# Performance work log

Hardware: AMD Instinct MI355X
Metric: run time of the kernel (lower is better)

## Reference

```python
import jax, jax.numpy as jnp
import numpy as np

B, N, D, L, NREPEAT = 32, 577, 384, 12, 4
H = 4 * D  # mlp hidden
EPS = 1e-6


def ln(x, w, b):
    mu = jnp.mean(x, axis=-1, keepdims=True)
    var = jnp.mean(jnp.square(x - mu), axis=-1, keepdims=True)
    return (x - mu) * jax.lax.rsqrt(var + EPS) * w + b


def setup_inputs() -> dict:
    key = jax.random.key(0)
    ks = jax.random.split(key, 16)
    s = 0.02
    return {
        "x": jax.random.normal(ks[0], (B, N, D), dtype=jnp.float32),
        "norm1_w": jnp.ones((L, D), jnp.float32),
        "norm1_b": jnp.zeros((L, D), jnp.float32),
        "qkv_w": jax.random.normal(ks[1], (L, 3 * D, D), jnp.float32) * s,
        "qkv_b": jnp.zeros((L, 3 * D), jnp.float32),
        "qn_w": jnp.ones((L, D), jnp.float32),
        "qn_b": jnp.zeros((L, D), jnp.float32),
        "kn_w": jnp.ones((L, D), jnp.float32),
        "kn_b": jnp.zeros((L, D), jnp.float32),
        "an_w": jnp.ones((L, D), jnp.float32),
        "an_b": jnp.zeros((L, D), jnp.float32),
        "proj_w": jax.random.normal(ks[2], (L, D, D), jnp.float32) * s,
        "proj_b": jnp.zeros((L, D), jnp.float32),
        "ls1": jnp.full((L, D), 1e-5, jnp.float32),
        "norm2_w": jnp.ones((L, D), jnp.float32),
        "norm2_b": jnp.zeros((L, D), jnp.float32),
        "fc1_w": jax.random.normal(ks[3], (L, H, D), jnp.float32) * s,
        "fc1_b": jnp.zeros((L, H), jnp.float32),
        "fc2_w": jax.random.normal(ks[4], (L, D, H), jnp.float32) * s,
        "fc2_b": jnp.zeros((L, D), jnp.float32),
        "ls2": jnp.full((L, D), 1e-5, jnp.float32),
    }


def _forward(x, norm1_w, norm1_b, qkv_w, qkv_b, qn_w, qn_b, kn_w, kn_b,
             an_w, an_b, proj_w, proj_b, ls1, norm2_w, norm2_b,
             fc1_w, fc1_b, fc2_w, fc2_b, ls2):
    scale = 1.0 / np.sqrt(D).astype(np.float32)
    x_prime = x
    history = []  # list of [B, 1, D] cls tokens, grows each repeat
    for _ in range(NREPEAT):
        new_cls = x[:, 0:1]
        x = jnp.concatenate([new_cls, x_prime[:, 1:]], axis=1)  # [B, N, D]
        mem = jnp.concatenate([x] + history, axis=1)            # [B, N+t, D]
        for l in range(L):
            res1 = x
            xn = ln(x, norm1_w[l], norm1_b[l])
            # manual qkv split: q from normed x, k/v from UNNORMED mem
            q = xn @ qkv_w[l, :D].T + qkv_b[l, :D]
            k = mem @ qkv_w[l, D:2 * D].T + qkv_b[l, D:2 * D]
            v = mem @ qkv_w[l, 2 * D:].T + qkv_b[l, 2 * D:]
            q = ln(q, qn_w[l], qn_b[l])
            k = ln(k, kn_w[l], kn_b[l])
            # single-head SDPA over full width D
            attn = jax.nn.softmax(jnp.einsum('bqd,bkd->bqk', q, k) * scale, axis=-1)
            prod = jnp.einsum('bqk,bkd->bqd', attn, v)
            prod = ln(prod, an_w[l], an_b[l])
            proj = prod @ proj_w[l].T + proj_b[l]
            x = proj * ls1[l] + res1
            res2 = x
            x2 = ln(x, norm2_w[l], norm2_b[l])
            h = jax.nn.gelu(x2 @ fc1_w[l].T + fc1_b[l], approximate=False)
            x1 = h @ fc2_w[l].T + fc2_b[l]
            x = x1 * ls2[l] + res2
        history.append(new_cls)
    return x


def reference(x, norm1_w, norm1_b, qkv_w, qkv_b, qn_w, qn_b, kn_w, kn_b,
              an_w, an_b, proj_w, proj_b, ls1, norm2_w, norm2_b,
              fc1_w, fc1_b, fc2_w, fc2_b, ls2):
    return _forward(x, norm1_w, norm1_b, qkv_w, qkv_b, qn_w, qn_b, kn_w, kn_b,
                    an_w, an_b, proj_w, proj_b, ls1, norm2_w, norm2_b,
                    fc1_w, fc1_b, fc2_w, fc2_b, ls2)
```

## Files before the change

### kernel.cpp

```cpp
#include <hip/hip_runtime.h>
#include <math.h>

#define BB 32
#define NN 577
#define DD 384
#define HD 1536
#define LL 12
#define MP 608
#define NRPT 4

typedef __attribute__((ext_vector_type(8))) short bf16x8;
typedef __attribute__((ext_vector_type(4))) float f32x4;

__device__ __forceinline__ unsigned short f2bf(float f){
  unsigned u = __builtin_bit_cast(unsigned, f);
  u += 0x7fffu + ((u >> 16) & 1u);
  return (unsigned short)(u >> 16);
}
__device__ __forceinline__ float bf2f(unsigned short s){
  unsigned u = ((unsigned)s) << 16;
  return __builtin_bit_cast(float, u);
}

__device__ __forceinline__ void async16(void* lds, const void* g){
  __builtin_amdgcn_global_load_lds(
      (const __attribute__((address_space(1))) unsigned int*)g,
      (__attribute__((address_space(3))) unsigned int*)lds, 16, 0, 0);
}


__global__ void reset_k(float* __restrict__ x, const float* __restrict__ xp, float* __restrict__ cls){
  int i = blockIdx.x * 256 + threadIdx.x;
  if (i >= BB*NN*DD) return;
  int d = i % DD;
  int n = (i / DD) % NN;
  int b = i / (NN*DD);
  if (n == 0) cls[b*DD + d] = x[i];
  else x[i] = xp[i];
}

__global__ void fillmem_k(const float* __restrict__ x, const float* __restrict__ cls_hist,
                          unsigned short* __restrict__ mem, int r){
  int i = blockIdx.x * 256 + threadIdx.x;
  if (i >= BB*MP*DD) return;
  int d = i % DD;
  int n = (i / DD) % MP;
  int b = i / (MP*DD);
  float v = 0.f;
  if (n < NN) v = x[((size_t)b*NN + n)*DD + d];
  else if (n < NN + r) v = cls_hist[(size_t)(n-NN)*BB*DD + b*DD + d];
  mem[i] = f2bf(v);
}

__global__ void castL_k(const float* __restrict__ qkvw, const float* __restrict__ pw,
                        const float* __restrict__ f1w, const float* __restrict__ f2w,
                        unsigned short* __restrict__ wbuf){
  int i = blockIdx.x * 256 + threadIdx.x;
  const int QKV = 3*DD*DD;
  const int PRJ = DD*DD;
  const int F1  = HD*DD;
  const int TOT = QKV + PRJ + 2*F1;
  if (i >= TOT) return;
  float v;
  if (i < QKV) v = qkvw[i];
  else if (i < QKV+PRJ) v = pw[i-QKV];
  else if (i < QKV+PRJ+F1) v = f1w[i-QKV-PRJ];
  else v = f2w[i-QKV-PRJ-F1];
  wbuf[i] = f2bf(v);
}


template<typename T>
__global__ __launch_bounds__(64) void ln_k(const T* __restrict__ in, const float* __restrict__ w,
                                           const float* __restrict__ bias, unsigned short* __restrict__ out){
  int row = blockIdx.x;
  int lane = threadIdx.x;
  const T* p = in + (size_t)row*DD;
  float v[6];
  float s = 0.f;
  #pragma unroll
  for (int i=0;i<6;i++){
    float t;
    if (sizeof(T) == 4) t = (float)p[lane + i*64];
    else t = bf2f((unsigned short)p[lane + i*64]);
    v[i] = t; s += t;
  }
  #pragma unroll
  for (int o=32;o;o>>=1) s += __shfl_xor(s, o, 64);
  float mu = s * (1.f/DD);
  float q = 0.f;
  #pragma unroll
  for (int i=0;i<6;i++){ float t = v[i]-mu; q += t*t; }
  #pragma unroll
  for (int o=32;o;o>>=1) q += __shfl_xor(q, o, 64);
  float rs = rsqrtf(q*(1.f/DD) + 1e-6f);
  unsigned short* po = out + (size_t)row*DD;
  #pragma unroll
  for (int i=0;i<6;i++){
    int c = lane + i*64;
    po[c] = f2bf((v[i]-mu)*rs*w[c] + bias[c]);
  }
}


template<int EPI>
__global__ __launch_bounds__(256) void gemm128(
    const unsigned short* __restrict__ A, int lda, int arows, long sA,
    const unsigned short* __restrict__ B, int ldb, int brows, long sB,
    const float* __restrict__ bias,
    int K, int N,
    float* __restrict__ outF, unsigned short* __restrict__ outB,
    int ldo, int orows, long sO,
    const float* __restrict__ ls){

  __shared__ unsigned short a_sh[128*32];
  __shared__ unsigned short b_sh[128*32];

  int tid  = threadIdx.x;
  int wave = tid >> 6, lane = tid & 63;
  int lr = lane & 15, kg = lane >> 4;
  int wm = wave >> 1, wn = wave & 1;
  int z = blockIdx.z;
  int row0 = blockIdx.y * 128;
  int col0 = blockIdx.x * 128;

  const unsigned short* Ab = A + (size_t)z*sA;
  const unsigned short* Bb = B + (size_t)z*sB;

  f32x4 zf = {0.f,0.f,0.f,0.f};
  f32x4 acc[4][4];
  #pragma unroll
  for (int i=0;i<4;i++)
    #pragma unroll
    for (int j=0;j<4;j++) acc[i][j] = zf;

  int ra[2], rb[2], kc[2];
  #pragma unroll
  for (int it=0; it<2; it++){
    int c = tid + it*256;
    int r = row0 + (c>>2); if (r > arows-1) r = arows-1;
    ra[it] = r;
    r = col0 + (c>>2); if (r > brows-1) r = brows-1;
    rb[it] = r;
    kc[it] = (c&3)*8;
  }

  for (int k0 = 0; k0 < K; k0 += 32){
    #pragma unroll
    for (int it=0; it<2; it++){
      unsigned short* la = &a_sh[(it*256 + wave*64)*8];
      unsigned short* lb = &b_sh[(it*256 + wave*64)*8];
      async16(la, Ab + (size_t)ra[it]*lda + k0 + kc[it]);
      async16(lb, Bb + (size_t)rb[it]*ldb + k0 + kc[it]);
    }
    __syncthreads();
    bf16x8 af[4], bf[4];
    #pragma unroll
    for (int i=0;i<4;i++){
      af[i] = *(const bf16x8*)&a_sh[(wm*64 + i*16 + lr)*32 + kg*8];
      bf[i] = *(const bf16x8*)&b_sh[(wn*64 + i*16 + lr)*32 + kg*8];
    }
    #pragma unroll
    for (int i=0;i<4;i++)
      #pragma unroll
      for (int j=0;j<4;j++)
        acc[i][j] = __builtin_amdgcn_mfma_f32_16x16x32_bf16(af[i], bf[j], acc[i][j], 0,0,0);
    __syncthreads();
  }

  float* oF = outF ? outF + (size_t)z*sO : nullptr;
  unsigned short* oB = outB ? outB + (size_t)z*sO : nullptr;

  #pragma unroll
  for (int mi=0;mi<4;mi++)
    #pragma unroll
    for (int ni=0;ni<4;ni++)
      #pragma unroll
      for (int r=0;r<4;r++){
        int row = row0 + wm*64 + mi*16 + kg*4 + r;
        int col = col0 + wn*64 + ni*16 + lr;
        if (row >= orows || col >= N) continue;
        float vv = acc[mi][ni][r];
        size_t idx = (size_t)row*ldo + col;
        if (EPI == 0){
          if (bias) vv += bias[col];
          oB[idx] = f2bf(vv);
        } else if (EPI == 1){
          vv += bias[row];
          oB[idx] = f2bf(vv);
        } else if (EPI == 2){
          vv += bias[col];
          oF[idx] = vv*ls[col] + oF[idx];
        } else {
          vv += bias[col];
          float g = 0.5f*vv*(1.f + erff(vv*0.70710678118f));
          oB[idx] = f2bf(g);
        }
      }
}

__global__ __launch_bounds__(64) void softmax_k(const unsigned short* __restrict__ S,
                                                unsigned short* __restrict__ P, int M){
  int row = blockIdx.x;
  int m = row % MP;
  int lane = threadIdx.x;
  unsigned short* po = P + (size_t)row*MP;
  if (m >= NN){
    for (int n = lane; n < MP; n += 64) po[n] = 0;
    return;
  }
  const unsigned short* ps = S + (size_t)row*MP;
  const float scale = 0.05103103588f;
  float t[10];
  float mx = -INFINITY;
  #pragma unroll
  for (int i=0;i<10;i++){
    int n = lane + i*64;
    float v = (n < M) ? bf2f(ps[n])*scale : -INFINITY;
    t[i] = v; mx = fmaxf(mx, v);
  }
  #pragma unroll
  for (int o=32;o;o>>=1) mx = fmaxf(mx, __shfl_xor(mx, o, 64));
  float s = 0.f;
  #pragma unroll
  for (int i=0;i<10;i++){
    int n = lane + i*64;
    float e = (n < M) ? expf(t[i]-mx) : 0.f;
    t[i] = e; s += e;
  }
  #pragma unroll
  for (int o=32;o;o>>=1) s += __shfl_xor(s, o, 64);
  float inv = 1.f / s;
  #pragma unroll
  for (int i=0;i<10;i++){
    int n = lane + i*64;
    if (n < MP) po[n] = f2bf(t[i]*inv);
  }
}


extern "C" void kernel_launch(void* const* d_in, const int* in_sizes, int n_in,
                              void* d_out, int out_size, void* d_ws, size_t ws_size,
                              hipStream_t stream){
  const float* x_in = (const float*)d_in[0];
  const float* n1w  = (const float*)d_in[1];
  const float* n1b  = (const float*)d_in[2];
  const float* qkvw = (const float*)d_in[3];
  const float* qkvb = (const float*)d_in[4];
  const float* qnw  = (const float*)d_in[5];
  const float* qnb  = (const float*)d_in[6];
  const float* knw  = (const float*)d_in[7];
  const float* knb  = (const float*)d_in[8];
  const float* anw  = (const float*)d_in[9];
  const float* anb  = (const float*)d_in[10];
  const float* pw   = (const float*)d_in[11];
  const float* pb   = (const float*)d_in[12];
  const float* ls1  = (const float*)d_in[13];
  const float* n2w  = (const float*)d_in[14];
  const float* n2b  = (const float*)d_in[15];
  const float* f1w  = (const float*)d_in[16];
  const float* f1b  = (const float*)d_in[17];
  const float* f2w  = (const float*)d_in[18];
  const float* f2bb = (const float*)d_in[19];
  const float* ls2  = (const float*)d_in[20];

  char* ws = (char*)d_ws;
  size_t off = 0;
  auto alloc = [&](size_t bytes)->char* {
    char* p = ws + off;
    off = (off + bytes + 255) & ~(size_t)255;
    return p;
  };

  const int QKV = 3*DD*DD, PRJ = DD*DD, F1 = HD*DD;
  const size_t WTOT = (size_t)QKV + PRJ + 2*F1;
  const size_t SLOT = (size_t)BB*MP*DD;

  unsigned short* wbuf  = (unsigned short*)alloc(WTOT*2);
  float*          cls_h = (float*)         alloc((size_t)NRPT*BB*DD*4);
  unsigned short* mem_bf= (unsigned short*)alloc(SLOT*2);
  unsigned short* pool  = (unsigned short*)alloc(6*SLOT*2);

  unsigned short* wq = wbuf;
  unsigned short* wp = wbuf + QKV;
  unsigned short* w1 = wbuf + QKV + PRJ;
  unsigned short* w2 = wbuf + QKV + PRJ + F1;

  unsigned short* S0 = pool;
  unsigned short* S1 = pool + SLOT;
  unsigned short* S2 = pool + 2*SLOT;
  unsigned short* S3 = pool + 3*SLOT;
  unsigned short* S4 = pool + 4*SLOT;
  unsigned short* S5 = pool + 5*SLOT;

  unsigned short* xn    = S0;
  unsigned short* qraw  = S1;
  unsigned short* kraw  = S2;
  unsigned short* qb    = S3;
  unsigned short* kb    = S4;
  unsigned short* vT    = S5;
  unsigned short* Ssc   = S1;
  unsigned short* Pbf   = S3;
  unsigned short* prod  = S0;
  unsigned short* prodn = S1;
  unsigned short* x2    = S0;
  unsigned short* h     = S1;

  float* xf = (float*)d_out;

  auto cg = [](size_t n){ return dim3((unsigned)((n + 255) / 256)); };

  hipMemcpyAsync(xf, x_in, (size_t)BB*NN*DD*4, hipMemcpyDeviceToDevice, stream);

  const int RT  = (BB*NN + 127)/128;
  const int RTM = (BB*MP)/128;

  for (int r = 0; r < NRPT; r++){
    int M = NN + r;
    reset_k<<<cg((size_t)BB*NN*DD),256,0,stream>>>(xf, x_in, cls_h + (size_t)r*BB*DD);
    fillmem_k<<<cg((size_t)BB*MP*DD),256,0,stream>>>(xf, cls_h, mem_bf, r);
    for (int l = 0; l < LL; l++){
      castL_k<<<cg(WTOT),256,0,stream>>>(qkvw + (size_t)l*QKV, pw + (size_t)l*PRJ,
                                         f1w + (size_t)l*F1, f2w + (size_t)l*F1, wbuf);
      ln_k<float><<<BB*NN,64,0,stream>>>(xf, n1w + l*DD, n1b + l*DD, xn);
      gemm128<0><<<dim3(3,RT,1),256,0,stream>>>(xn,384,BB*NN,0, wq,384,384,0,
          qkvb + l*3*DD, 384,384, nullptr,qraw,384,BB*NN,0, nullptr);
      gemm128<0><<<dim3(3,RTM,1),256,0,stream>>>(mem_bf,384,BB*MP,0, wq + (size_t)DD*DD,384,384,0,
          qkvb + l*3*DD + DD, 384,384, nullptr,kraw,384,BB*MP,0, nullptr);
      gemm128<1><<<dim3(5,3,BB),256,0,stream>>>(wq + (size_t)2*DD*DD,384,384,0, mem_bf,384,MP,(long)MP*DD,
          qkvb + l*3*DD + 2*DD, 384,MP, nullptr,vT,MP,384,(long)DD*MP, nullptr);
      ln_k<unsigned short><<<BB*NN,64,0,stream>>>(qraw, qnw + l*DD, qnb + l*DD, qb);
      ln_k<unsigned short><<<BB*MP,64,0,stream>>>(kraw, knw + l*DD, knb + l*DD, kb);
      gemm128<0><<<dim3(5,5,BB),256,0,stream>>>(qb,384,NN,(long)NN*DD, kb,384,MP,(long)MP*DD,
          nullptr, 384,MP, nullptr,Ssc,MP,NN,(long)MP*MP, nullptr);
      softmax_k<<<BB*MP,64,0,stream>>>(Ssc, Pbf, M);
      gemm128<0><<<dim3(3,5,BB),256,0,stream>>>(Pbf,MP,MP,(long)MP*MP, vT,MP,DD,(long)DD*MP,
          nullptr, MP,DD, nullptr,prod,DD,NN,(long)NN*DD, nullptr);
      ln_k<unsigned short><<<BB*NN,64,0,stream>>>(prod, anw + l*DD, anb + l*DD, prodn);
      gemm128<2><<<dim3(3,RT,1),256,0,stream>>>(prodn,384,BB*NN,0, wp,384,384,0,
          pb + l*DD, 384,384, xf,nullptr,384,BB*NN,0, ls1 + l*DD);
      ln_k<float><<<BB*NN,64,0,stream>>>(xf, n2w + l*DD, n2b + l*DD, x2);
      gemm128<3><<<dim3(12,RT,1),256,0,stream>>>(x2,384,BB*NN,0, w1,384,HD,0,
          f1b + l*HD, 384,HD, nullptr,h,HD,BB*NN,0, nullptr);
      gemm128<2><<<dim3(3,RT,1),256,0,stream>>>(h,HD,BB*NN,0, w2,HD,384,0,
          f2bb + l*DD, HD,384, xf,nullptr,384,BB*NN,0, ls2 + l*DD);
    }
  }
}
```

Baseline: 18.46 ms.

## Merge prep kernels, pack LN/softmax rows, unroll GEMM K loop, pad MP to 640

Merges the reset and memory-fill kernels into one prep kernel, runs layernorm and softmax with four rows per 256-thread block, and loads two 32-wide K slices per barrier pair in the GEMM. The sequence padding is raised to 640 so attention dimensions divide evenly by the 128 tile. This targets barrier overhead, tiny-block launch inefficiency and extra passes, at the cost of doubled LDS use and some extra padded attention work.

```diff
diff --git a/kernel.cpp b/kernel.cpp
--- a/kernel.cpp
+++ b/kernel.cpp
@@ -6,7 +6,7 @@
 #define DD 384
 #define HD 1536
 #define LL 12
-#define MP 608
+#define MP 640
 #define NRPT 4
 
 typedef __attribute__((ext_vector_type(8))) short bf16x8;
@@ -28,27 +28,19 @@
       (__attribute__((address_space(3))) unsigned int*)lds, 16, 0, 0);
 }
 
-
-__global__ void reset_k(float* __restrict__ x, const float* __restrict__ xp, float* __restrict__ cls){
-  int i = blockIdx.x * 256 + threadIdx.x;
-  if (i >= BB*NN*DD) return;
-  int d = i % DD;
-  int n = (i / DD) % NN;
-  int b = i / (NN*DD);
-  if (n == 0) cls[b*DD + d] = x[i];
-  else x[i] = xp[i];
-}
-
-__global__ void fillmem_k(const float* __restrict__ x, const float* __restrict__ cls_hist,
-                          unsigned short* __restrict__ mem, int r){
+__global__ void prep_k(float* __restrict__ x, const float* __restrict__ xp,
+                       float* __restrict__ cls_r, const float* __restrict__ cls_hist,
+                       unsigned short* __restrict__ mem, int r){
   int i = blockIdx.x * 256 + threadIdx.x;
   if (i >= BB*MP*DD) return;
   int d = i % DD;
   int n = (i / DD) % MP;
   int b = i / (MP*DD);
-  float v = 0.f;
-  if (n < NN) v = x[((size_t)b*NN + n)*DD + d];
-  else if (n < NN + r) v = cls_hist[(size_t)(n-NN)*BB*DD + b*DD + d];
+  float v;
+  if (n == 0){ v = x[(size_t)b*NN*DD + d]; cls_r[b*DD + d] = v; }
+  else if (n < NN){ v = xp[((size_t)b*NN + n)*DD + d]; x[((size_t)b*NN + n)*DD + d] = v; }
+  else if (n < NN + r){ v = cls_hist[(size_t)(n-NN)*BB*DD + b*DD + d]; }
+  else v = 0.f;
   mem[i] = f2bf(v);
 }
 
@@ -69,12 +61,13 @@
   wbuf[i] = f2bf(v);
 }
 
-
 template<typename T>
-__global__ __launch_bounds__(64) void ln_k(const T* __restrict__ in, const float* __restrict__ w,
-                                           const float* __restrict__ bias, unsigned short* __restrict__ out){
-  int row = blockIdx.x;
-  int lane = threadIdx.x;
+__global__ __launch_bounds__(256) void ln4_k(const T* __restrict__ in, const float* __restrict__ w,
+                                             const float* __restrict__ bias, unsigned short* __restrict__ out,
+                                             int nrows){
+  int row = blockIdx.x*4 + (threadIdx.x >> 6);
+  if (row >= nrows) return;
+  int lane = threadIdx.x & 63;
   const T* p = in + (size_t)row*DD;
   float v[6];
   float s = 0.f;
@@ -113,8 +106,8 @@
     int ldo, int orows, long sO,
     const float* __restrict__ ls){
 
-  __shared__ unsigned short a_sh[128*32];
-  __shared__ unsigned short b_sh[128*32];
+  __shared__ unsigned short a_sh[2][128*32];
+  __shared__ unsigned short b_sh[2][128*32];
 
   int tid  = threadIdx.x;
   int wave = tid >> 6, lane = tid & 63;
@@ -145,26 +138,32 @@
     kc[it] = (c&3)*8;
   }
 
-  for (int k0 = 0; k0 < K; k0 += 32){
+  for (int k0 = 0; k0 < K; k0 += 64){
     #pragma unroll
-    for (int it=0; it<2; it++){
-      unsigned short* la = &a_sh[(it*256 + wave*64)*8];
-      unsigned short* lb = &b_sh[(it*256 + wave*64)*8];
-      async16(la, Ab + (size_t)ra[it]*lda + k0 + kc[it]);
-      async16(lb, Bb + (size_t)rb[it]*ldb + k0 + kc[it]);
+    for (int p=0;p<2;p++){
+      #pragma unroll
+      for (int it=0; it<2; it++){
+        unsigned short* la = &a_sh[p][(it*256 + wave*64)*8];
+        unsigned short* lb = &b_sh[p][(it*256 + wave*64)*8];
+        async16(la, Ab + (size_t)ra[it]*lda + k0 + p*32 + kc[it]);
+        async16(lb, Bb + (size_t)rb[it]*ldb + k0 + p*32 + kc[it]);
+      }
     }
     __syncthreads();
-    bf16x8 af[4], bf[4];
     #pragma unroll
-    for (int i=0;i<4;i++){
-      af[i] = *(const bf16x8*)&a_sh[(wm*64 + i*16 + lr)*32 + kg*8];
-      bf[i] = *(const bf16x8*)&b_sh[(wn*64 + i*16 + lr)*32 + kg*8];
+    for (int p=0;p<2;p++){
+      bf16x8 af[4], bfr[4];
+      #pragma unroll
+      for (int i=0;i<4;i++){
+        af[i]  = *(const bf16x8*)&a_sh[p][(wm*64 + i*16 + lr)*32 + kg*8];
+        bfr[i] = *(const bf16x8*)&b_sh[p][(wn*64 + i*16 + lr)*32 + kg*8];
+      }
+      #pragma unroll
+      for (int i=0;i<4;i++)
+        #pragma unroll
+        for (int j=0;j<4;j++)
+          acc[i][j] = __builtin_amdgcn_mfma_f32_16x16x32_bf16(af[i], bfr[j], acc[i][j], 0,0,0);
     }
-    #pragma unroll
-    for (int i=0;i<4;i++)
-      #pragma unroll
-      for (int j=0;j<4;j++)
-        acc[i][j] = __builtin_amdgcn_mfma_f32_16x16x32_bf16(af[i], bf[j], acc[i][j], 0,0,0);
     __syncthreads();
   }
 
@@ -199,11 +198,11 @@
       }
 }
 
-__global__ __launch_bounds__(64) void softmax_k(const unsigned short* __restrict__ S,
-                                                unsigned short* __restrict__ P, int M){
-  int row = blockIdx.x;
+__global__ __launch_bounds__(256) void softmax4_k(const unsigned short* __restrict__ S,
+                                                  unsigned short* __restrict__ P, int M){
+  int row = blockIdx.x*4 + (threadIdx.x >> 6);
   int m = row % MP;
-  int lane = threadIdx.x;
+  int lane = threadIdx.x & 63;
   unsigned short* po = P + (size_t)row*MP;
   if (m >= NN){
     for (int n = lane; n < MP; n += 64) po[n] = 0;
@@ -234,7 +233,7 @@
   #pragma unroll
   for (int i=0;i<10;i++){
     int n = lane + i*64;
-    if (n < MP) po[n] = f2bf(t[i]*inv);
+    po[n] = f2bf(t[i]*inv);
   }
 }
 
@@ -312,38 +311,39 @@
 
   hipMemcpyAsync(xf, x_in, (size_t)BB*NN*DD*4, hipMemcpyDeviceToDevice, stream);
 
-  const int RT  = (BB*NN + 127)/128;
-  const int RTM = (BB*MP)/128;
+  const int RT   = (BB*NN + 127)/128;
+  const int RTM  = (BB*MP)/128;
+  const int QR   = BB*NN;
+  const int KR   = BB*MP;
 
   for (int r = 0; r < NRPT; r++){
     int M = NN + r;
-    reset_k<<<cg((size_t)BB*NN*DD),256,0,stream>>>(xf, x_in, cls_h + (size_t)r*BB*DD);
-    fillmem_k<<<cg((size_t)BB*MP*DD),256,0,stream>>>(xf, cls_h, mem_bf, r);
+    prep_k<<<cg((size_t)BB*MP*DD),256,0,stream>>>(xf, x_in, cls_h + (size_t)r*BB*DD, cls_h, mem_bf, r);
     for (int l = 0; l < LL; l++){
       castL_k<<<cg(WTOT),256,0,stream>>>(qkvw + (size_t)l*QKV, pw + (size_t)l*PRJ,
                                          f1w + (size_t)l*F1, f2w + (size_t)l*F1, wbuf);
-      ln_k<float><<<BB*NN,64,0,stream>>>(xf, n1w + l*DD, n1b + l*DD, xn);
-      gemm128<0><<<dim3(3,RT,1),256,0,stream>>>(xn,384,BB*NN,0, wq,384,384,0,
-          qkvb + l*3*DD, 384,384, nullptr,qraw,384,BB*NN,0, nullptr);
-      gemm128<0><<<dim3(3,RTM,1),256,0,stream>>>(mem_bf,384,BB*MP,0, wq + (size_t)DD*DD,384,384,0,
-          qkvb + l*3*DD + DD, 384,384, nullptr,kraw,384,BB*MP,0, nullptr);
-      gemm128<1><<<dim3(5,3,BB),256,0,stream>>>(wq + (size_t)2*DD*DD,384,384,0, mem_bf,384,MP,(long)MP*DD,
+      ln4_k<float><<<cg((size_t)QR*64),256,0,stream>>>(xf, n1w + l*DD, n1b + l*DD, xn, QR);
+      gemm128<0><<<dim3(3,RT,1),256,0,stream>>>(xn,384,QR,0, wq,384,384,0,
+          qkvb + l*3*DD, 384,384, nullptr,qraw,384,QR,0, nullptr);
+      gemm128<0><<<dim3(3,RTM,1),256,0,stream>>>(mem_bf,384,KR,0, wq + (size_t)DD*DD,384,384,0,
+          qkvb + l*3*DD + DD, 384,384, nullptr,kraw,384,KR,0, nullptr);
+      gemm128<1><<<dim3(MP/128,3,BB),256,0,stream>>>(wq + (size_t)2*DD*DD,384,384,0, mem_bf,384,MP,(long)MP*DD,
           qkvb + l*3*DD + 2*DD, 384,MP, nullptr,vT,MP,384,(long)DD*MP, nullptr);
-      ln_k<unsigned short><<<BB*NN,64,0,stream>>>(qraw, qnw + l*DD, qnb + l*DD, qb);
-      ln_k<unsigned short><<<BB*MP,64,0,stream>>>(kraw, knw + l*DD, knb + l*DD, kb);
-      gemm128<0><<<dim3(5,5,BB),256,0,stream>>>(qb,384,NN,(long)NN*DD, kb,384,MP,(long)MP*DD,
+      ln4_k<unsigned short><<<cg((size_t)QR*64),256,0,stream>>>(qraw, qnw + l*DD, qnb + l*DD, qb, QR);
+      ln4_k<unsigned short><<<cg((size_t)KR*64),256,0,stream>>>(kraw, knw + l*DD, knb + l*DD, kb, KR);
+      gemm128<0><<<dim3(MP/128,MP/128,BB),256,0,stream>>>(qb,384,NN,(long)NN*DD, kb,384,MP,(long)MP*DD,
           nullptr, 384,MP, nullptr,Ssc,MP,NN,(long)MP*MP, nullptr);
-      softmax_k<<<BB*MP,64,0,stream>>>(Ssc, Pbf, M);
-      gemm128<0><<<dim3(3,5,BB),256,0,stream>>>(Pbf,MP,MP,(long)MP*MP, vT,MP,DD,(long)DD*MP,
+      softmax4_k<<<KR/4,256,0,stream>>>(Ssc, Pbf, M);
+      gemm128<0><<<dim3(3,MP/128,BB),256,0,stream>>>(Pbf,MP,MP,(long)MP*MP, vT,MP,DD,(long)DD*MP,
           nullptr, MP,DD, nullptr,prod,DD,NN,(long)NN*DD, nullptr);
-      ln_k<unsigned short><<<BB*NN,64,0,stream>>>(prod, anw + l*DD, anb + l*DD, prodn);
-      gemm128<2><<<dim3(3,RT,1),256,0,stream>>>(prodn,384,BB*NN,0, wp,384,384,0,
-          pb + l*DD, 384,384, xf,nullptr,384,BB*NN,0, ls1 + l*DD);
-      ln_k<float><<<BB*NN,64,0,stream>>>(xf, n2w + l*DD, n2b + l*DD, x2);
-      gemm128<3><<<dim3(12,RT,1),256,0,stream>>>(x2,384,BB*NN,0, w1,384,HD,0,
-          f1b + l*HD, 384,HD, nullptr,h,HD,BB*NN,0, nullptr);
-      gemm128<2><<<dim3(3,RT,1),256,0,stream>>>(h,HD,BB*NN,0, w2,HD,384,0,
-          f2bb + l*DD, HD,384, xf,nullptr,384,BB*NN,0, ls2 + l*DD);
+      ln4_k<unsigned short><<<cg((size_t)QR*64),256,0,stream>>>(prod, anw + l*DD, anb + l*DD, prodn, QR);
+      gemm128<2><<<dim3(3,RT,1),256,0,stream>>>(prodn,384,QR,0, wp,384,384,0,
+          pb + l*DD, 384,384, xf,nullptr,384,QR,0, ls1 + l*DD);
+      ln4_k<float><<<cg((size_t)QR*64),256,0,stream>>>(xf, n2w + l*DD, n2b + l*DD, x2, QR);
+      gemm128<3><<<dim3(HD/128,RT,1),256,0,stream>>>(x2,384,QR,0, w1,384,HD,0,
+          f1b + l*HD, 384,HD, nullptr,h,HD,QR,0, nullptr);
+      gemm128<2><<<dim3(3,RT,1),256,0,stream>>>(h,HD,QR,0, w2,HD,384,0,
+          f2bb + l*DD, HD,384, xf,nullptr,384,QR,0, ls2 + l*DD);
     }
   }
 }
```

Measured after the change: 17.30 ms. 6.3% less time.
